# Optimization experiments

Measured on AMD Instinct MI355X. Metric: run time of the kernel, lower is better.

## Reference

```python
import jax, jax.numpy as jnp
import numpy as np


def l2norm(t, eps=1e-12):
    # matches F.normalize(p=2, dim=-1): divide by norm clamped to eps
    n = jnp.linalg.norm(t, axis=-1, keepdims=True)
    return t / jnp.maximum(n, eps)


def setup_inputs() -> dict:
    key = jax.random.key(0)
    kx, ke = jax.random.split(key)
    B, N, D, C = 8, 1024, 256, 8192
    x = jax.random.normal(kx, (B, N, D), dtype=jnp.float32)
    # codebook initialized l2-normalized, as in __init__ (kmeans_init=False)
    embed = l2norm(jax.random.normal(ke, (1, C, D), dtype=jnp.float32))
    return {"x": x, "embed": embed}


def reference(x, embed):
    # x: [B, N, D]; ndim < 4 -> add codebook dim h=1
    xh = x[None]                                   # [1, B, N, D]
    h, b, n, d = xh.shape
    flat = l2norm(xh.reshape(h, b * n, d))         # [1, B*N, D]
    e = l2norm(embed)                              # [1, C, D]
    # cosine-similarity distances
    dist = jnp.einsum('hnd,hcd->hnc', flat, e)     # [1, B*N, C]
    # sample_codebook_temp == 0 -> plain argmax
    idx = jnp.argmax(dist, axis=-1).reshape(h, b, n)  # [1, B, N]
    # batched_embedding: gather UN-normalized codebook rows
    quantize = jax.vmap(lambda em, ix: em[ix])(embed, idx)  # [1, B, N, D]
    # needs_codebook_dim -> strip leading dim
    return quantize[0], idx[0]
```

## Files before the change

kernel.cpp:

```cpp
#include <hip/hip_runtime.h>
#include <math.h>

#define QROWS 8192
#define DDIM  256
#define CCNT  8192

typedef __attribute__((ext_vector_type(4))) float f32x4;
typedef __attribute__((ext_vector_type(8))) short bf16x8;

__device__ __forceinline__ unsigned short f2bf(float f) {
    unsigned u = __float_as_uint(f);
    u += 0x7fffu + ((u >> 16) & 1u);
    return (unsigned short)(u >> 16);
}
__device__ __forceinline__ unsigned u32max(unsigned a, unsigned b) { return a > b ? a : b; }
__device__ __forceinline__ unsigned u32min(unsigned a, unsigned b) { return a < b ? a : b; }

__device__ __forceinline__ unsigned key32(float v, unsigned enc) {
    return ((__float_as_uint(v) ^ 0x80000000u) & 0xFFFFFF00u) | enc;
}

__global__ void k_prep(const float* __restrict__ x, unsigned short* __restrict__ xb,
                       const float* __restrict__ e, unsigned short* __restrict__ eb) {
    const int bid = blockIdx.x;
    if (bid < 1024) {
        const int i = (bid * 256 + threadIdx.x) * 8;
        const float4 f0 = *reinterpret_cast<const float4*>(x + i);
        const float4 f1 = *reinterpret_cast<const float4*>(x + i + 4);
        uint4 o;
        o.x = f2bf(f0.x) | ((unsigned)f2bf(f0.y) << 16);
        o.y = f2bf(f0.z) | ((unsigned)f2bf(f0.w) << 16);
        o.z = f2bf(f1.x) | ((unsigned)f2bf(f1.y) << 16);
        o.w = f2bf(f1.z) | ((unsigned)f2bf(f1.w) << 16);
        *reinterpret_cast<uint4*>(xb + i) = o;
    } else {
        const int row  = (bid - 1024) * 4 + (threadIdx.x >> 6);
        const int lane = threadIdx.x & 63;
        const float4 v = *reinterpret_cast<const float4*>(e + (size_t)row * DDIM + lane * 4);
        float s = v.x * v.x + v.y * v.y + v.z * v.z + v.w * v.w;
        #pragma unroll
        for (int off = 1; off < 64; off <<= 1) s += __shfl_xor(s, off);
        const float inv = 1.0f / fmaxf(sqrtf(s), 1e-12f);
        ushort4 o;
        o.x = f2bf(v.x * inv); o.y = f2bf(v.y * inv);
        o.z = f2bf(v.z * inv); o.w = f2bf(v.w * inv);
        *reinterpret_cast<ushort4*>(eb + (size_t)row * DDIM + lane * 4) = o;
    }
}

#define GLOAD_LDS(g, s) \
    __builtin_amdgcn_global_load_lds((const __attribute__((address_space(1))) void*)(g), \
                                     (__attribute__((address_space(3))) void*)(s), 16, 0, 0)

#define SBAR do { asm volatile("" ::: "memory"); __builtin_amdgcn_s_barrier(); \
                  asm volatile("" ::: "memory"); } while (0)
#define WAIT_LGKM(n) do { asm volatile("s_waitcnt lgkmcnt(" #n ")" ::: "memory"); \
                          __builtin_amdgcn_sched_barrier(0); } while (0)
#define WAIT_VM(n) do { asm volatile("s_waitcnt vmcnt(" #n ")" ::: "memory"); \
                        __builtin_amdgcn_sched_barrier(0); } while (0)

__launch_bounds__(256, 2)
__global__ void k_gemm(const unsigned short* __restrict__ xb,
                       const unsigned short* __restrict__ eb,
                       unsigned* pout ) {
    extern __shared__ char smem[];

    const int tid = threadIdx.x;
    const int w = tid >> 6, l = tid & 63;
    const int lg = l >> 4, lr = l & 15, lr7 = lr & 7;
    const int bid = blockIdx.x;
    const int q = bid >> 3;
    const int panel = (bid & 7) * 4 + (q >> 4);
    const int split = q & 15;
    const int n0 = panel * 256, c0 = split * 512;

    const int lchk = (tid & 24) | ((tid & 7) ^ ((tid >> 5) & 7));
    const char* baseA = (const char*)xb + (size_t)(n0 + (tid >> 5)) * 512 + lchk * 16;
    const char* baseB = (const char*)eb + (size_t)(c0 + (tid >> 5)) * 512 + lchk * 16;
    const int wl16 = w * 1024;

#define STAGE_AROUND(r) do { _Pragma("unroll") for (int g_ = 0; g_ < 16; ++g_)             \
    GLOAD_LDS(baseA + (r) * 65536 + g_ * 4096, smem + g_ * 4096 + wl16); } while (0)
#define STAGEB(t) do { _Pragma("unroll") for (int g_ = 0; g_ < 2; ++g_)                    \
    GLOAD_LDS(baseB + (size_t)(t) * 8192 + g_ * 4096,                                      \
              smem + ((t) & 7) * 8192 + g_ * 4096 + wl16); } while (0)

    bf16x8 aF[4][8];
#define READA() do { _Pragma("unroll") for (int mi_ = 0; mi_ < 4; ++mi_)                   \
    _Pragma("unroll") for (int kk_ = 0; kk_ < 8; ++kk_) {                                  \
        const int lc_ = kk_ * 4 + lg;                                                      \
        const int ph_ = (lc_ & 24) | ((lc_ & 7) ^ lr7);                                    \
        aF[mi_][kk_] = *reinterpret_cast<const bf16x8*>(                                   \
            smem + ((w & 1) * 64 + mi_ * 16 + lr) * 512 + ph_ * 16); } } while (0)

    STAGE_AROUND(0);
    WAIT_VM(0); SBAR;
    if (w < 2) READA();
    WAIT_LGKM(0); SBAR;
    STAGE_AROUND(1);
    WAIT_VM(0); SBAR;
    if (w >= 2) READA();
    WAIT_LGKM(0); SBAR;
    STAGEB(0); STAGEB(1); STAGEB(2); STAGEB(3); STAGEB(4); STAGEB(5);

    const f32x4 zf4 = {0.f, 0.f, 0.f, 0.f};
    unsigned rk1[16], rk2[16];
    #pragma unroll
    for (int i = 0; i < 16; ++i) { rk1[i] = 0u; rk2[i] = 0u; }

#define TILE(t) do {                                                                       \
    const char* sb_ = smem + ((t) & 7) * 8192;                                             \
    f32x4 ac_[4];                                                                          \
    {                                                                                      \
        const int ph0_ = ((lg & 24) | ((lg & 7) ^ lr7)) * 16;                              \
        const bf16x8 b_ = *reinterpret_cast<const bf16x8*>(sb_ + lr * 512 + ph0_);         \
        _Pragma("unroll") for (int mi_ = 0; mi_ < 4; ++mi_)                                \
            ac_[mi_] = __builtin_amdgcn_mfma_f32_16x16x32_bf16(aF[mi_][0], b_, zf4, 0, 0, 0); \
    }                                                                                      \
    _Pragma("unroll") for (int kk_ = 1; kk_ < 8; ++kk_) {                                  \
        const int lc_ = kk_ * 4 + lg;                                                      \
        const int ph_ = ((lc_ & 24) | ((lc_ & 7) ^ lr7)) * 16;                             \
        const bf16x8 b_ = *reinterpret_cast<const bf16x8*>(sb_ + lr * 512 + ph_);          \
        _Pragma("unroll") for (int mi_ = 0; mi_ < 4; ++mi_)                                \
            ac_[mi_] = __builtin_amdgcn_mfma_f32_16x16x32_bf16(aF[mi_][kk_], b_, ac_[mi_], 0, 0, 0); \
    }                                                                                      \
    const unsigned encb_ = (unsigned)(255 - ((t) & 15) * 16) - (unsigned)lr;               \
    _Pragma("unroll") for (int mi_ = 0; mi_ < 4; ++mi_)                                    \
        _Pragma("unroll") for (int rr_ = 0; rr_ < 4; ++rr_) {                              \
            const unsigned q_ = key32(ac_[mi_][rr_], encb_);                               \
            const int i_ = mi_ * 4 + rr_;                                                  \
            const unsigned lo_ = u32min(rk1[i_], q_);                                      \
            rk1[i_] = u32max(rk1[i_], q_);                                                 \
            rk2[i_] = u32max(rk2[i_], lo_);                                                \
        }                                                                                  \
} while (0)

#define FLUSH(half) do {                                                                   \
    _Pragma("unroll") for (int i_ = 0; i_ < 16; ++i_) {                                    \
        unsigned t1_ = rk1[i_], t2_ = rk2[i_];                                             \
        _Pragma("unroll") for (int off_ = 1; off_ < 16; off_ <<= 1) {                      \
            const unsigned o1_ = __shfl_xor(t1_, off_);                                    \
            const unsigned o2_ = __shfl_xor(t2_, off_);                                    \
            const unsigned n1_ = u32max(t1_, o1_), lo_ = u32min(t1_, o1_);                 \
            t2_ = u32max(u32max(t2_, o2_), lo_);                                           \
            t1_ = n1_;                                                                     \
        }                                                                                  \
        if (lr == 0) {                                                                     \
            const int row_ = n0 + w * 64 + (i_ >> 2) * 16 + lg * 4 + (i_ & 3);             \
            uint2 o_; o_.x = t1_; o_.y = t2_;                                              \
            *reinterpret_cast<uint2*>(pout + (size_t)row_ * 256 + split * 4 + (half) * 2) = o_; \
        }                                                                                  \
        rk1[i_] = 0u; rk2[i_] = 0u;                                                        \
    }                                                                                      \
} while (0)

    #pragma unroll 1
    for (int u = 0; u < 16; ++u) {
        if (u < 14)      { WAIT_VM(8); }
        else if (u == 14){ WAIT_VM(4); }
        else             { WAIT_VM(0); }
        SBAR;
        if (u < 13) { STAGEB(2 * u + 6); STAGEB(2 * u + 7); }
        TILE(2 * u);
        TILE(2 * u + 1);
        if (u == 7)  FLUSH(0);
        if (u == 15) FLUSH(1);
    }
#undef STAGE_AROUND
#undef STAGEB
#undef READA
#undef TILE
#undef FLUSH
}

__global__ void k_fixup(const unsigned* pk,
                        const float* __restrict__ x, const float* __restrict__ e,
                        float* out) {
    const int row = blockIdx.x * 4 + (threadIdx.x >> 6);
    const int t   = threadIdx.x & 63;
    unsigned long long kk0 = 0ull, kk1 = 0ull;
    if (t < 32) {
        const uint2 kv = reinterpret_cast<const uint2*>(pk + (size_t)row * 256)[t];
        const int col0 = t * 256 + 255 - (int)(kv.x & 255u);
        kk0 = ((unsigned long long)(kv.x & 0xFFFFFF00u) << 32) | (unsigned)(~col0);
        const int col1 = t * 256 + 255 - (int)(kv.y & 255u);
        kk1 = ((unsigned long long)(kv.y & 0xFFFFFF00u) << 32) | (unsigned)(~col1);
    }

    int cand[4];
    #pragma unroll
    for (int p = 0; p < 4; ++p) {
        unsigned long long m = kk0 > kk1 ? kk0 : kk1;
        #pragma unroll
        for (int off = 1; off < 64; off <<= 1) {
            const unsigned long long o = __shfl_xor(m, off);
            if (o > m) m = o;
        }
        cand[p] = (int)(~(unsigned)m) & (CCNT - 1);
        if (kk0 == m) kk0 = 0ull;
        if (kk1 == m) kk1 = 0ull;
    }

    const float4 xv = *reinterpret_cast<const float4*>(x + (size_t)row * DDIM + t * 4);
    float best = -INFINITY; int bc = 0x7fffffff;
    #pragma unroll
    for (int p = 0; p < 4; ++p) {
        const int c = cand[p];
        const float4 ev = *reinterpret_cast<const float4*>(e + (size_t)c * DDIM + t * 4);
        float d  = xv.x * ev.x + xv.y * ev.y + xv.z * ev.z + xv.w * ev.w;
        float ss = ev.x * ev.x + ev.y * ev.y + ev.z * ev.z + ev.w * ev.w;
        #pragma unroll
        for (int off = 1; off < 64; off <<= 1) {
            d  += __shfl_xor(d, off);
            ss += __shfl_xor(ss, off);
        }
        const float v = d * (1.0f / fmaxf(sqrtf(ss), 1e-12f));
        if (v > best || (v == best && c < bc)) { best = v; bc = c; }
    }

    if (t == 0) out[(size_t)QROWS * DDIM + row] = (float)bc;
    const float4 qv = *reinterpret_cast<const float4*>(e + (size_t)bc * DDIM + t * 4);
    *reinterpret_cast<float4*>(out + (size_t)row * DDIM + t * 4) = qv;
}

extern "C" void kernel_launch(void* const* d_in, const int* in_sizes, int n_in,
                              void* d_out, int out_size, void* d_ws, size_t ws_size,
                              hipStream_t stream) {
    const float* x = (const float*)d_in[0];
    const float* e = (const float*)d_in[1];
    float* out = (float*)d_out;
    char* ws = (char*)d_ws;

    unsigned short* xb = (unsigned short*)ws;
    unsigned short* eb = (unsigned short*)(ws + (size_t)4 * 1024 * 1024);

    hipFuncSetAttribute(reinterpret_cast<const void*>(k_gemm),
                        hipFuncAttributeMaxDynamicSharedMemorySize, 65536);

    k_prep<<<3072, 256, 0, stream>>>(x, xb, e, eb);
    k_gemm<<<512, 256, 65536, stream>>>(xb, eb, (unsigned*)d_out);
    k_fixup<<<QROWS / 4, 256, 0, stream>>>((const unsigned*)d_out, x, e, out);
}
```

Baseline: 61.09 us.

## Halve GEMM row tile, load A fragments directly to registers, raise occupancy

The GEMM block now covers 128 query rows instead of 256, so 1024 blocks launch. A fragments are loaded straight from global memory into registers rather than staged through LDS. The B ring buffer drops from 8 to 6 stages (48KB LDS), launch bounds rise to 3 blocks per CU, and the main loop is fully unrolled. This aims to cut register and LDS pressure and the serialized A-staging prologue for better occupancy, at the cost of less reuse of each B tile across rows (twice the B traffic) and a shallower prefetch depth.

```diff
diff --git a/kernel.cpp b/kernel.cpp
--- a/kernel.cpp
+++ b/kernel.cpp
@@ -54,12 +54,10 @@
 
 #define SBAR do { asm volatile("" ::: "memory"); __builtin_amdgcn_s_barrier(); \
                   asm volatile("" ::: "memory"); } while (0)
-#define WAIT_LGKM(n) do { asm volatile("s_waitcnt lgkmcnt(" #n ")" ::: "memory"); \
-                          __builtin_amdgcn_sched_barrier(0); } while (0)
 #define WAIT_VM(n) do { asm volatile("s_waitcnt vmcnt(" #n ")" ::: "memory"); \
                         __builtin_amdgcn_sched_barrier(0); } while (0)
 
-__launch_bounds__(256, 2)
+__launch_bounds__(256, 3)
 __global__ void k_gemm(const unsigned short* __restrict__ xb,
                        const unsigned short* __restrict__ eb,
                        unsigned* pout ) {
@@ -69,74 +67,67 @@
     const int w = tid >> 6, l = tid & 63;
     const int lg = l >> 4, lr = l & 15, lr7 = lr & 7;
     const int bid = blockIdx.x;
-    const int q = bid >> 3;
-    const int panel = (bid & 7) * 4 + (q >> 4);
-    const int split = q & 15;
-    const int n0 = panel * 256, c0 = split * 512;
+    const int X = bid & 7, loc = bid >> 3;
+    const int split = (X * 2 + (loc >> 6)) & 15;
+    const int rg = loc & 63;
+    const int n0 = rg * 128, c0 = split * 512;
+
+    bf16x8 aF[2][8];
+    {
+        const char* gA = (const char*)xb + (size_t)(n0 + w * 32 + lr) * 512 + lg * 16;
+        #pragma unroll
+        for (int mi = 0; mi < 2; ++mi)
+            #pragma unroll
+            for (int kk = 0; kk < 8; ++kk)
+                aF[mi][kk] = *reinterpret_cast<const bf16x8*>(gA + mi * 16 * 512 + kk * 64);
+    }
 
     const int lchk = (tid & 24) | ((tid & 7) ^ ((tid >> 5) & 7));
-    const char* baseA = (const char*)xb + (size_t)(n0 + (tid >> 5)) * 512 + lchk * 16;
     const char* baseB = (const char*)eb + (size_t)(c0 + (tid >> 5)) * 512 + lchk * 16;
     const int wl16 = w * 1024;
 
-#define STAGE_AROUND(r) do { _Pragma("unroll") for (int g_ = 0; g_ < 16; ++g_)             \
-    GLOAD_LDS(baseA + (r) * 65536 + g_ * 4096, smem + g_ * 4096 + wl16); } while (0)
 #define STAGEB(t) do { _Pragma("unroll") for (int g_ = 0; g_ < 2; ++g_)                    \
     GLOAD_LDS(baseB + (size_t)(t) * 8192 + g_ * 4096,                                      \
-              smem + ((t) & 7) * 8192 + g_ * 4096 + wl16); } while (0)
-
-    bf16x8 aF[4][8];
-#define READA() do { _Pragma("unroll") for (int mi_ = 0; mi_ < 4; ++mi_)                   \
-    _Pragma("unroll") for (int kk_ = 0; kk_ < 8; ++kk_) {                                  \
-        const int lc_ = kk_ * 4 + lg;                                                      \
-        const int ph_ = (lc_ & 24) | ((lc_ & 7) ^ lr7);                                    \
-        aF[mi_][kk_] = *reinterpret_cast<const bf16x8*>(                                   \
-            smem + ((w & 1) * 64 + mi_ * 16 + lr) * 512 + ph_ * 16); } } while (0)
-
-    STAGE_AROUND(0);
-    WAIT_VM(0); SBAR;
-    if (w < 2) READA();
-    WAIT_LGKM(0); SBAR;
-    STAGE_AROUND(1);
-    WAIT_VM(0); SBAR;
-    if (w >= 2) READA();
-    WAIT_LGKM(0); SBAR;
-    STAGEB(0); STAGEB(1); STAGEB(2); STAGEB(3); STAGEB(4); STAGEB(5);
+              smem + ((t) % 6) * 8192 + g_ * 4096 + wl16); } while (0)
+
+    STAGEB(0); STAGEB(1); STAGEB(2); STAGEB(3);
 
     const f32x4 zf4 = {0.f, 0.f, 0.f, 0.f};
-    unsigned rk1[16], rk2[16];
-    #pragma unroll
-    for (int i = 0; i < 16; ++i) { rk1[i] = 0u; rk2[i] = 0u; }
+    unsigned rk1[8], rk2[8];
+    #pragma unroll
+    for (int i = 0; i < 8; ++i) { rk1[i] = 0u; rk2[i] = 0u; }
 
 #define TILE(t) do {                                                                       \
-    const char* sb_ = smem + ((t) & 7) * 8192;                                             \
-    f32x4 ac_[4];                                                                          \
+    const char* sb_ = smem + ((t) % 6) * 8192;                                             \
+    f32x4 ac0_, ac1_;                                                                      \
     {                                                                                      \
         const int ph0_ = ((lg & 24) | ((lg & 7) ^ lr7)) * 16;                              \
         const bf16x8 b_ = *reinterpret_cast<const bf16x8*>(sb_ + lr * 512 + ph0_);         \
-        _Pragma("unroll") for (int mi_ = 0; mi_ < 4; ++mi_)                                \
-            ac_[mi_] = __builtin_amdgcn_mfma_f32_16x16x32_bf16(aF[mi_][0], b_, zf4, 0, 0, 0); \
+        ac0_ = __builtin_amdgcn_mfma_f32_16x16x32_bf16(aF[0][0], b_, zf4, 0, 0, 0);        \
+        ac1_ = __builtin_amdgcn_mfma_f32_16x16x32_bf16(aF[1][0], b_, zf4, 0, 0, 0);        \
     }                                                                                      \
     _Pragma("unroll") for (int kk_ = 1; kk_ < 8; ++kk_) {                                  \
         const int lc_ = kk_ * 4 + lg;                                                      \
         const int ph_ = ((lc_ & 24) | ((lc_ & 7) ^ lr7)) * 16;                             \
         const bf16x8 b_ = *reinterpret_cast<const bf16x8*>(sb_ + lr * 512 + ph_);          \
-        _Pragma("unroll") for (int mi_ = 0; mi_ < 4; ++mi_)                                \
-            ac_[mi_] = __builtin_amdgcn_mfma_f32_16x16x32_bf16(aF[mi_][kk_], b_, ac_[mi_], 0, 0, 0); \
+        ac0_ = __builtin_amdgcn_mfma_f32_16x16x32_bf16(aF[0][kk_], b_, ac0_, 0, 0, 0);     \
+        ac1_ = __builtin_amdgcn_mfma_f32_16x16x32_bf16(aF[1][kk_], b_, ac1_, 0, 0, 0);     \
     }                                                                                      \
     const unsigned encb_ = (unsigned)(255 - ((t) & 15) * 16) - (unsigned)lr;               \
-    _Pragma("unroll") for (int mi_ = 0; mi_ < 4; ++mi_)                                    \
-        _Pragma("unroll") for (int rr_ = 0; rr_ < 4; ++rr_) {                              \
-            const unsigned q_ = key32(ac_[mi_][rr_], encb_);                               \
-            const int i_ = mi_ * 4 + rr_;                                                  \
-            const unsigned lo_ = u32min(rk1[i_], q_);                                      \
-            rk1[i_] = u32max(rk1[i_], q_);                                                 \
-            rk2[i_] = u32max(rk2[i_], lo_);                                                \
-        }                                                                                  \
+    _Pragma("unroll") for (int rr_ = 0; rr_ < 4; ++rr_) {                                  \
+        const unsigned q0_ = key32(ac0_[rr_], encb_);                                      \
+        const unsigned lo0_ = u32min(rk1[rr_], q0_);                                       \
+        rk1[rr_] = u32max(rk1[rr_], q0_);                                                  \
+        rk2[rr_] = u32max(rk2[rr_], lo0_);                                                 \
+        const unsigned q1_ = key32(ac1_[rr_], encb_);                                      \
+        const unsigned lo1_ = u32min(rk1[4 + rr_], q1_);                                   \
+        rk1[4 + rr_] = u32max(rk1[4 + rr_], q1_);                                          \
+        rk2[4 + rr_] = u32max(rk2[4 + rr_], lo1_);                                         \
+    }                                                                                      \
 } while (0)
 
 #define FLUSH(half) do {                                                                   \
-    _Pragma("unroll") for (int i_ = 0; i_ < 16; ++i_) {                                    \
+    _Pragma("unroll") for (int i_ = 0; i_ < 8; ++i_) {                                     \
         unsigned t1_ = rk1[i_], t2_ = rk2[i_];                                             \
         _Pragma("unroll") for (int off_ = 1; off_ < 16; off_ <<= 1) {                      \
             const unsigned o1_ = __shfl_xor(t1_, off_);                                    \
@@ -146,7 +137,7 @@
             t1_ = n1_;                                                                     \
         }                                                                                  \
         if (lr == 0) {                                                                     \
-            const int row_ = n0 + w * 64 + (i_ >> 2) * 16 + lg * 4 + (i_ & 3);             \
+            const int row_ = n0 + w * 32 + (i_ >> 2) * 16 + lg * 4 + (i_ & 3);             \
             uint2 o_; o_.x = t1_; o_.y = t2_;                                              \
             *reinterpret_cast<uint2*>(pout + (size_t)row_ * 256 + split * 4 + (half) * 2) = o_; \
         }                                                                                  \
@@ -154,21 +145,20 @@
     }                                                                                      \
 } while (0)
 
-    #pragma unroll 1
+    WAIT_VM(4); SBAR;
+    #pragma unroll
     for (int u = 0; u < 16; ++u) {
-        if (u < 14)      { WAIT_VM(8); }
-        else if (u == 14){ WAIT_VM(4); }
-        else             { WAIT_VM(0); }
-        SBAR;
-        if (u < 13) { STAGEB(2 * u + 6); STAGEB(2 * u + 7); }
+        if (u >= 1) {
+            if (u < 15) { WAIT_VM(4); } else { WAIT_VM(0); }
+            SBAR;
+        }
+        if (u <= 13) { STAGEB(2 * u + 4); STAGEB(2 * u + 5); }
         TILE(2 * u);
         TILE(2 * u + 1);
         if (u == 7)  FLUSH(0);
         if (u == 15) FLUSH(1);
     }
-#undef STAGE_AROUND
 #undef STAGEB
-#undef READA
 #undef TILE
 #undef FLUSH
 }
@@ -235,9 +225,9 @@
     unsigned short* eb = (unsigned short*)(ws + (size_t)4 * 1024 * 1024);
 
     hipFuncSetAttribute(reinterpret_cast<const void*>(k_gemm),
-                        hipFuncAttributeMaxDynamicSharedMemorySize, 65536);
+                        hipFuncAttributeMaxDynamicSharedMemorySize, 49152);
 
     k_prep<<<3072, 256, 0, stream>>>(x, xb, e, eb);
-    k_gemm<<<512, 256, 65536, stream>>>(xb, eb, (unsigned*)d_out);
+    k_gemm<<<1024, 256, 49152, stream>>>(xb, eb, (unsigned*)d_out);
     k_fixup<<<QROWS / 4, 256, 0, stream>>>((const unsigned*)d_out, x, e, out);
 }
```

Result: slower. 101.1 us (+65.4%).
